# Kernel optimization log

Hardware: AMD Instinct MI355X
Metric: run time of the kernel (lower is better)

The kernel has to match this reference:

```python
import jax, jax.numpy as jnp
import numpy as np

WINDOW_SIZE = 11
SIGMA = 1.5
CHANNEL = 3
L = 2.0
C1 = (0.01 * L) ** 2
C2 = (0.03 * L) ** 2
WEIGHTS = jnp.asarray([0.0448, 0.2856, 0.3001, 0.2363, 0.1333], dtype=jnp.float32)


def _create_window(window_size=WINDOW_SIZE, channel=CHANNEL):
    x = jnp.arange(window_size, dtype=jnp.float32)
    g = jnp.exp(-((x - window_size // 2) ** 2) / (2.0 * SIGMA ** 2))
    g = g / g.sum()
    w2d = jnp.outer(g, g)  # (ws, ws)
    # depthwise kernel, OIHW with I=1, O=channel
    return jnp.broadcast_to(w2d[None, None], (channel, 1, window_size, window_size))


def _depthwise_conv(x, w):
    # x: (B,C,H,W), w: (C,1,kh,kw), groups=C, VALID padding
    return jax.lax.conv_general_dilated(
        x, w, window_strides=(1, 1), padding='VALID',
        feature_group_count=x.shape[1],
        dimension_numbers=('NCHW', 'OIHW', 'NCHW'))


def _ssim_level(img1, img2, window):
    mu1 = _depthwise_conv(img1, window)
    mu2 = _depthwise_conv(img2, window)
    mu1_sq = mu1 * mu1
    mu2_sq = mu2 * mu2
    mu1_mu2 = mu1 * mu2
    sigma1_sq = _depthwise_conv(img1 * img1, window) - mu1_sq
    sigma2_sq = _depthwise_conv(img2 * img2, window) - mu2_sq
    sigma12 = _depthwise_conv(img1 * img2, window) - mu1_mu2
    v1 = 2.0 * sigma12 + C2
    v2 = sigma1_sq + sigma2_sq + C2
    cs = jnp.mean(v1 / v2)
    ssim_map = (2.0 * mu1_mu2 + C1) * v1 / ((mu1_sq + mu2_sq + C1) * v2)
    return jnp.mean(ssim_map), cs


def _avg_pool2(x):
    b, c, h, w = x.shape
    return x.reshape(b, c, h // 2, 2, w // 2, 2).mean(axis=(3, 5))


def _msssim(img1, img2):
    window = _create_window()
    mssim, mcs = [], []
    for _ in range(WEIGHTS.shape[0]):
        sim, cs = _ssim_level(img1, img2, window)
        mssim.append(sim)
        mcs.append(cs)
        img1 = _avg_pool2(img1)
        img2 = _avg_pool2(img2)
    mssim = jnp.stack(mssim)
    mcs = jnp.stack(mcs)
    # normalize=True
    mssim = (mssim + 1.0) / 2.0
    mcs = (mcs + 1.0) / 2.0
    pow1 = mcs ** WEIGHTS
    pow2 = mssim ** WEIGHTS
    # faithful to source: prod over broadcast of pow1[:-1] * pow2[-1]
    return jnp.prod(pow1[:-1] * pow2[-1])


def setup_inputs() -> dict:
    key = jax.random.key(0)
    k1, k2 = jax.random.split(key)
    shape = (16, 3, 512, 512)
    output = jax.random.uniform(k1, shape, dtype=jnp.float32)
    gt = jax.random.uniform(k2, shape, dtype=jnp.float32)
    return {"output": output, "gt": gt}


def reference(output, gt):
    return 1.0 - _msssim(output, gt)
```

## Files before the change

kernel.cpp:

```cpp
#include <hip/hip_runtime.h>
#include <math.h>

typedef float vf2 __attribute__((ext_vector_type(2)));

__device__ __forceinline__ vf2 pk_fma(vf2 a, vf2 b, vf2 c) {
    vf2 d;
    asm("v_pk_fma_f32 %0, %1, %2, %3" : "=v"(d) : "v"(a), "v"(b), "v"(c));
    return d;
}
__device__ __forceinline__ vf2 pk_mul(vf2 a, vf2 b) {
    vf2 d;
    asm("v_pk_mul_f32 %0, %1, %2" : "=v"(d) : "v"(a), "v"(b));
    return d;
}
__device__ __forceinline__ vf2 pk_fma_blo(vf2 w, vf2 b, vf2 c) {
    vf2 d;
    asm("v_pk_fma_f32 %0, %1, %2, %3 op_sel_hi:[0,1,1]"
        : "=v"(d) : "v"(w), "v"(b), "v"(c));
    return d;
}
__device__ __forceinline__ vf2 pk_fma_bhi(vf2 w, vf2 b, vf2 c) {
    vf2 d;
    asm("v_pk_fma_f32 %0, %1, %2, %3 op_sel:[1,0,0] op_sel_hi:[1,1,1]"
        : "=v"(d) : "v"(w), "v"(b), "v"(c));
    return d;
}

#define L0_H 512
#define L0_HOUT 502
#define L0_HP 256
#define L0_SEG 64
#define L0_NCHUNK 7
#define ROWW 536
#define NQ 134
#define BUF_WORDS (11 * ROWW)
#define CARRY0 (2 * BUF_WORDS)
#define STREAM_WORDS (CARRY0 + 2 * ROWW)

__global__ __launch_bounds__(256)
void msssim_stream_l0(const float* __restrict__ img1,
                      const float* __restrict__ img2,
                      double* __restrict__ sums,
                      float* __restrict__ poolP, float* __restrict__ poolQ)
{
    __shared__ __align__(16) float buf[STREAM_WORDS];
    __shared__ float wred[4][2];

    const float gs[11] = {0.00102838f, 0.00759875f, 0.03600077f, 0.10936070f,
                          0.21300554f, 0.26601173f, 0.21300554f, 0.10936070f,
                          0.03600077f, 0.00759875f, 0.00102838f};

    const int tid = threadIdx.x;
    const int c0 = blockIdx.x * 256;
    const int oy0 = blockIdx.y * L0_SEG;
    const long long plane = (long long)blockIdx.z * L0_H * L0_H;
    const long long pplane = (long long)blockIdx.z * L0_HP * L0_HP;
    const bool colok = (c0 + tid) < L0_HOUT;

    const int par = tid & 1;
    vf2 wp[6];
    #pragma unroll
    for (int jq = 0; jq < 6; ++jq) {
        const int i0 = 2 * jq, i1 = 2 * jq + 1;
        const float we0 = (i0 < 11) ? gs[i0] : 0.f;
        const float wo0 = (i0 >= 1) ? gs[i0 - 1] : 0.f;
        const float we1 = (i1 < 11) ? gs[i1] : 0.f;
        const float wo1 = (i1 >= 1) ? gs[i1 - 1] : 0.f;
        wp[jq].x = par ? wo0 : we0;
        wp[jq].y = par ? wo1 : we1;
    }
    vf2 wgv[6];
    #pragma unroll
    for (int k = 0; k < 6; ++k) { wgv[k].x = gs[k]; wgv[k].y = gs[k]; }

    int rowS[6], colS[6], ldsoff[6], rHS[6];
    #pragma unroll
    for (int t = 0; t < 6; ++t) {
        const int s = tid + 256 * t;
        if (s < 11 * NQ) {
            const int r = s / NQ, q = s - NQ * r;
            rowS[t] = r;
            colS[t] = c0 + 2 * q;
            ldsoff[t] = r * ROWW + q * 4;
            rHS[t] = r * L0_H;
        } else { rowS[t] = -1; colS[t] = 0; ldsoff[t] = 0; rHS[t] = 0; }
    }

    float4 pf[6];
    auto prefetch = [&](int ybase) {
        const int yH = ybase * L0_H;
        #pragma unroll
        for (int t = 0; t < 6; ++t) {
            float2 a = make_float2(0.f, 0.f), b = make_float2(0.f, 0.f);
            if (rowS[t] >= 0) {
                const int y = ybase + rowS[t];
                if (y < L0_H && colS[t] < L0_H) {
                    const long long idx = plane + yH + rHS[t] + colS[t];
                    a = *(const float2*)(img1 + idx);
                    b = *(const float2*)(img2 + idx);
                }
            }
            pf[t] = make_float4(a.x + b.x, a.x - b.x, a.y + b.y, a.y - b.y);
        }
    };
    auto stage_write = [&](int base) {
        #pragma unroll
        for (int t = 0; t < 6; ++t)
            if (rowS[t] >= 0) *(float4*)&buf[base + ldsoff[t]] = pf[t];
    };

    prefetch(oy0);
    stage_write(0);
    __syncthreads();

    vf2 pd_pq[11], pd_sq[11];
    #pragma unroll
    for (int s = 0; s < 11; ++s) { pd_pq[s] = (vf2){0.f, 0.f}; pd_sq[s] = (vf2){0.f, 0.f}; }

    const int qb4 = (tid >> 1) * 4;
    const float C1 = 4.0e-4f, C2 = 3.6e-3f;
    float ssim_acc = 0.f, cs_acc = 0.f;

    for (int c = 0; c < L0_NCHUNK; ++c) {
        const int cs = oy0 + 11 * c;
        const bool more = (c + 1 < L0_NCHUNK);
        const int cb = (c & 1) * BUF_WORDS;
        const int nb = ((c + 1) & 1) * BUF_WORDS;

        if (more) prefetch(cs + 11);

        if (tid < 128) {
            const int px = (c0 >> 1) + tid;
            const int t4 = tid * 4;
            for (int jp = (cs & 1); jp + 1 <= 10; jp += 2) {
                const int py = (cs + jp) >> 1;
                if (py < L0_HP) {
                    const float4 v0 = *(const float4*)&buf[cb + jp * ROWW + t4];
                    const float4 v1 = *(const float4*)&buf[cb + (jp + 1) * ROWW + t4];
                    poolP[pplane + py * L0_HP + px] = 0.25f * (v0.x + v0.z + v1.x + v1.z);
                    poolQ[pplane + py * L0_HP + px] = 0.25f * (v0.y + v0.w + v1.y + v1.w);
                }
            }
            if (c > 0 && (cs & 1)) {
                const int py = (cs - 1) >> 1;
                if (py < L0_HP) {
                    const float4 v0 = *(const float4*)&buf[CARRY0 + ((c - 1) & 1) * ROWW + t4];
                    const float4 v1 = *(const float4*)&buf[cb + t4];
                    poolP[pplane + py * L0_HP + px] = 0.25f * (v0.x + v0.z + v1.x + v1.z);
                    poolQ[pplane + py * L0_HP + px] = 0.25f * (v0.y + v0.w + v1.y + v1.w);
                }
            }
        }
        if (((cs & 1) == 0) && more && tid < NQ) {
            *(float4*)&buf[CARRY0 + (c & 1) * ROWW + tid * 4] =
                *(const float4*)&buf[cb + 10 * ROWW + tid * 4];
        }

        #pragma unroll
        for (int j = 0; j < 11; ++j) {
            pd_pq[j] = (vf2){0.f, 0.f};
            pd_sq[j] = (vf2){0.f, 0.f};

            float4 q[6];
            const int rw = cb + j * ROWW + qb4;
            #pragma unroll
            for (int u = 0; u < 6; ++u) q[u] = *(const float4*)&buf[rw + 4 * u];

            vf2 hpq = {0.f, 0.f}, hsq = {0.f, 0.f};
            #pragma unroll
            for (int u = 0; u < 6; ++u) {
                const vf2 elo = {q[u].x, q[u].y};
                const vf2 ehi = {q[u].z, q[u].w};
                const vf2 slo = pk_mul(elo, elo);
                const vf2 shi = pk_mul(ehi, ehi);
                hpq = pk_fma_blo(wp[u], elo, hpq);
                hpq = pk_fma_bhi(wp[u], ehi, hpq);
                hsq = pk_fma_blo(wp[u], slo, hsq);
                hsq = pk_fma_bhi(wp[u], shi, hsq);
            }
            #pragma unroll
            for (int k = 0; k < 11; ++k) {
                const int s = (j - k + 11) % 11;
                const int m = (k <= 5) ? k : 10 - k;
                pd_pq[s] = pk_fma(wgv[m], hpq, pd_pq[s]);
                pd_sq[s] = pk_fma(wgv[m], hsq, pd_sq[s]);
            }
            const int yrel = 11 * c + j;
            if (yrel >= 10) {
                const int s = (j + 1) % 11;
                const int orow = yrel - 10;
                if (orow < L0_SEG && (oy0 + orow) < L0_HOUT && colok) {
                    const vf2 musq = pk_mul(pd_pq[s], pd_pq[s]);
                    const float sP = pd_sq[s].x - musq.x;
                    const float sQ = pd_sq[s].y - musq.y;
                    const float v1 = 0.5f * (sP - sQ) + C2;
                    const float v2 = 0.5f * (sP + sQ) + C2;
                    const float num1 = 0.5f * (musq.x - musq.y) + C1;
                    const float den1 = 0.5f * (musq.x + musq.y) + C1;
                    cs_acc += v1 * __builtin_amdgcn_rcpf(v2);
                    ssim_acc += num1 * v1 * __builtin_amdgcn_rcpf(den1 * v2);
                }
            }
        }

        if (more) stage_write(nb);
        __syncthreads();
    }

    #pragma unroll
    for (int off = 32; off > 0; off >>= 1) {
        ssim_acc += __shfl_down(ssim_acc, off);
        cs_acc   += __shfl_down(cs_acc, off);
    }
    const int wave = tid >> 6;
    if ((tid & 63) == 0) { wred[wave][0] = ssim_acc; wred[wave][1] = cs_acc; }
    __syncthreads();
    if (tid == 0) {
        atomicAdd(&sums[0], (double)(wred[0][0] + wred[1][0] + wred[2][0] + wred[3][0]));
        atomicAdd(&sums[5], (double)(wred[0][1] + wred[1][1] + wred[2][1] + wred[3][1]));
    }
}

#define TILE 32
#define IN_DIM 42
#define SCP 21
#define HALO 10
#define STAGE_WORDS (IN_DIM * SCP * 4)
#define SH 340
#define HB STAGE_WORDS
#define SMEM_WORDS (HB + 16 * SH)

__global__ __launch_bounds__(256)
void msssim_level_kernel(const float* __restrict__ src1,
                         const float* __restrict__ src2,
                         int H, int level, int tiles_per_seg, int pq_input,
                         double* __restrict__ sums,
                         float* __restrict__ pool1, float* __restrict__ pool2)
{
    __shared__ __align__(16) float smem[SMEM_WORDS];
    __shared__ float wred[4][2];

    const float g[11] = {0.00102838f, 0.00759875f, 0.03600077f, 0.10936070f,
                         0.21300554f, 0.26601173f, 0.21300554f, 0.10936070f,
                         0.03600077f, 0.00759875f, 0.00102838f};
    vf2 wg[11];
    #pragma unroll
    for (int k = 0; k < 11; ++k) { wg[k].x = g[k]; wg[k].y = g[k]; }

    const int tid = threadIdx.x;
    const int Hout = H - HALO;
    const int ntiles = (Hout + TILE - 1) / TILE;
    const int tstart = blockIdx.y * tiles_per_seg;
    const int tend = min(ntiles, tstart + tiles_per_seg);
    const int ox0 = blockIdx.x * TILE;
    const int Hp = H >> 1;
    const long long base = (long long)blockIdx.z * H * H;

    int rHS[4], rS[4], xS[4];
    #pragma unroll
    for (int t4 = 0; t4 < 4; ++t4) {
        const int s = tid + 256 * t4;
        if (s < IN_DIM * SCP) {
            const int r = s / SCP, cp = s - r * SCP;
            rS[t4] = r; rHS[t4] = r * H; xS[t4] = ox0 + 2 * cp;
        } else { rS[t4] = -1; rHS[t4] = 0; xS[t4] = 0; }
    }

    auto load_slot = [&](int t4, int ybase) -> float4 {
        float2 a = make_float2(0.f, 0.f), b = make_float2(0.f, 0.f);
        if (rS[t4] >= 0) {
            const int y = ybase + rS[t4], x = xS[t4];
            if (y < H && x < H) {
                const long long idx = base + (long long)ybase * H + rHS[t4] + x;
                a = *(const float2*)(src1 + idx);
                b = *(const float2*)(src2 + idx);
            }
        }
        if (pq_input) return make_float4(a.x, b.x, a.y, b.y);
        return make_float4(a.x + b.x, a.x - b.x, a.y + b.y, a.y - b.y);
    };

    float4 pref[4];
    {
        #pragma unroll
        for (int t4 = 0; t4 < 4; ++t4) pref[t4] = load_slot(t4, tstart * TILE);
        #pragma unroll
        for (int t4 = 0; t4 < 4; ++t4)
            if (rS[t4] >= 0) *(float4*)&smem[(tid + 256 * t4) * 4] = pref[t4];
    }
    __syncthreads();

    float ssim_acc = 0.f, cs_acc = 0.f;

    for (int tt = tstart; tt < tend; ++tt) {
        const int ty0 = tt * TILE;
        const bool more = (tt + 1 < tend);

        if (more) {
            #pragma unroll
            for (int t4 = 0; t4 < 4; ++t4) pref[t4] = load_slot(t4, ty0 + TILE);
        }

        if (pool1 != nullptr) {
            const int pr = tid >> 4, pc = tid & 15;
            const int py = (ty0 >> 1) + pr, px = (ox0 >> 1) + pc;
            if (py < Hp && px < Hp) {
                const float4 v0 = *(const float4*)&smem[(2 * pr * SCP + pc) * 4];
                const float4 v1 = *(const float4*)&smem[((2 * pr + 1) * SCP + pc) * 4];
                const long long ob = (long long)blockIdx.z * Hp * Hp + (long long)py * Hp + px;
                pool1[ob] = 0.25f * (v0.x + v0.z + v1.x + v1.z);
                pool2[ob] = 0.25f * (v0.y + v0.w + v1.y + v1.w);
            }
        }

        float4 hA[3], hBv[3];
        #pragma unroll
        for (int t = 0; t < 3; ++t) {
            const int p = tid + 256 * t;
            if (p < IN_DIM * 16) {
                const int r = p >> 4, m = p & 15;
                vf2 Apq = {0.f, 0.f}, Asq = {0.f, 0.f};
                vf2 Bpq = {0.f, 0.f}, Bsq = {0.f, 0.f};
                #pragma unroll
                for (int jj = 0; jj < 6; ++jj) {
                    const float4 v = *(const float4*)&smem[(r * SCP + m + jj) * 4];
                    const vf2 lo = {v.x, v.y};
                    const vf2 hi = {v.z, v.w};
                    const vf2 losq = pk_mul(lo, lo);
                    const vf2 hisq = pk_mul(hi, hi);
                    Apq = pk_fma(wg[2 * jj], lo, Apq);
                    Asq = pk_fma(wg[2 * jj], losq, Asq);
                    if (jj >= 1) {
                        Bpq = pk_fma(wg[2 * jj - 1], lo, Bpq);
                        Bsq = pk_fma(wg[2 * jj - 1], losq, Bsq);
                    }
                    if (jj <= 4) {
                        Apq = pk_fma(wg[2 * jj + 1], hi, Apq);
                        Asq = pk_fma(wg[2 * jj + 1], hisq, Asq);
                    }
                    Bpq = pk_fma(wg[2 * jj], hi, Bpq);
                    Bsq = pk_fma(wg[2 * jj], hisq, Bsq);
                }
                hA[t]  = make_float4(Apq.x, Apq.y, Asq.x, Asq.y);
                hBv[t] = make_float4(Bpq.x, Bpq.y, Bsq.x, Bsq.y);
            }
        }
        __syncthreads();

        #pragma unroll
        for (int t = 0; t < 3; ++t) {
            const int p = tid + 256 * t;
            if (p < IN_DIM * 16) {
                const int r = p >> 4, m = p & 15;
                const int hb = HB + m * SH + r * 8;
                *(float4*)&smem[hb]     = hA[t];
                *(float4*)&smem[hb + 4] = hBv[t];
            }
        }
        if (more) {
            #pragma unroll
            for (int t4 = 0; t4 < 4; ++t4)
                if (rS[t4] >= 0) *(float4*)&smem[(tid + 256 * t4) * 4] = pref[t4];
        }
        __syncthreads();

        const int tx = tid & 31, rg = tid >> 5;
        const int r0 = rg * 4;
        const int m = tx >> 1, par = tx & 1;
        const int hb = HB + m * SH + par * 4;

        vf2 accPQ[4], accSQ[4];
        #pragma unroll
        for (int o = 0; o < 4; ++o) {
            accPQ[o] = (vf2){0.f, 0.f};
            accSQ[o] = (vf2){0.f, 0.f};
        }
        #pragma unroll
        for (int i = 0; i < 14; ++i) {
            const float4 h4 = *(const float4*)&smem[hb + (r0 + i) * 8];
            const vf2 ppq = {h4.x, h4.y};
            const vf2 psq = {h4.z, h4.w};
            #pragma unroll
            for (int o = 0; o < 4; ++o) {
                const int k = i - o;
                if (k >= 0 && k <= 10) {
                    accPQ[o] = pk_fma(wg[k], ppq, accPQ[o]);
                    accSQ[o] = pk_fma(wg[k], psq, accSQ[o]);
                }
            }
        }

        const float C1 = 4.0e-4f;
        const float C2 = 3.6e-3f;
        const int ox = ox0 + tx;
        #pragma unroll
        for (int o = 0; o < 4; ++o) {
            const int oy = ty0 + r0 + o;
            if (oy < Hout && ox < Hout) {
                const vf2 musq = pk_mul(accPQ[o], accPQ[o]);
                const float sP = accSQ[o].x - musq.x;
                const float sQ = accSQ[o].y - musq.y;
                const float v1 = 0.5f * (sP - sQ) + C2;
                const float v2 = 0.5f * (sP + sQ) + C2;
                const float num1 = 0.5f * (musq.x - musq.y) + C1;
                const float den1 = 0.5f * (musq.x + musq.y) + C1;
                cs_acc += v1 * __builtin_amdgcn_rcpf(v2);
                ssim_acc += num1 * v1 * __builtin_amdgcn_rcpf(den1 * v2);
            }
        }
    }

    #pragma unroll
    for (int off = 32; off > 0; off >>= 1) {
        ssim_acc += __shfl_down(ssim_acc, off);
        cs_acc   += __shfl_down(cs_acc, off);
    }
    const int wave = tid >> 6;
    if ((tid & 63) == 0) { wred[wave][0] = ssim_acc; wred[wave][1] = cs_acc; }
    __syncthreads();
    if (tid == 0) {
        const float s = wred[0][0] + wred[1][0] + wred[2][0] + wred[3][0];
        const float c = wred[0][1] + wred[1][1] + wred[2][1] + wred[3][1];
        atomicAdd(&sums[level],     (double)s);
        atomicAdd(&sums[5 + level], (double)c);
    }
}

__global__ void msssim_final_kernel(const double* __restrict__ sums,
                                    float* __restrict__ out)
{
    if (threadIdx.x == 0 && blockIdx.x == 0) {
        const double W[5] = {0.0448, 0.2856, 0.3001, 0.2363, 0.1333};
        const int Houts[5] = {502, 246, 118, 54, 22};
        double mssim[5], mcs[5];
        for (int l = 0; l < 5; ++l) {
            const double cnt = 48.0 * (double)Houts[l] * (double)Houts[l];
            mssim[l] = (sums[l]     / cnt + 1.0) * 0.5;
            mcs[l]   = (sums[5 + l] / cnt + 1.0) * 0.5;
        }
        const double p2 = pow(mssim[4], W[4]);
        double prod = 1.0;
        for (int l = 0; l < 4; ++l) prod *= pow(mcs[l], W[l]) * p2;
        out[0] = (float)(1.0 - prod);
    }
}

extern "C" void kernel_launch(void* const* d_in, const int* in_sizes, int n_in,
                              void* d_out, int out_size, void* d_ws, size_t ws_size,
                              hipStream_t stream)
{
    const float* img1 = (const float*)d_in[0];
    const float* img2 = (const float*)d_in[1];
    float* out = (float*)d_out;
    (void)in_sizes; (void)n_in; (void)out_size; (void)ws_size;

    char* ws = (char*)d_ws;
    double* sums = (double*)ws;
    float* X1 = (float*)(ws + 256);
    float* X2 = X1 + 3145728;
    float* Y1 = X2 + 3145728;
    float* Y2 = Y1 + 786432;

    hipMemsetAsync(sums, 0, 10 * sizeof(double), stream);

    hipLaunchKernelGGL(msssim_stream_l0, dim3(2, 8, 48), dim3(256), 0, stream,
                       img1, img2, sums, X1, X2);

    auto launch_level = [&](const float* a, const float* b, int H, int level,
                            int segs, float* pa, float* pb) {
        const int Hout = H - HALO;
        const int strips = (Hout + TILE - 1) / TILE;
        const int ntiles = (Hout + TILE - 1) / TILE;
        const int tps = (ntiles + segs - 1) / segs;
        dim3 grid(strips, segs, 48);
        hipLaunchKernelGGL(msssim_level_kernel, grid, dim3(256), 0, stream,
                           a, b, H, level, tps, 1, sums, pa, pb);
    };

    launch_level(X1, X2, 256, 1, 2, Y1, Y2);
    launch_level(Y1, Y2, 128, 2, 4, X1, X2);
    launch_level(X1, X2, 64, 3, 2, Y1, Y2);
    launch_level(Y1, Y2, 32, 4, 1, nullptr, nullptr);

    hipLaunchKernelGGL(msssim_final_kernel, dim3(1), dim3(64), 0, stream, sums, out);
}
```

Measured before the change: 139.8 us.

## Precompute pyramid in one pool kernel and fuse levels 1-4 into one launch

A new kernel builds all downsampled levels (128, 64, 32) from the level-1 buffers in one pass per plane using LDS. The four per-level SSIM launches are then merged into a single launch whose blocks pick their level, strip and segment from a flat block index. The goal is to remove the serial dependency chain and the launch gaps between the small levels, so that the tiny levels run alongside level 1 and fill the GPU. The cost is an extra pool kernel with only 96 blocks, which may run with low occupancy, plus re-reading the level-1 data.

```diff
diff --git a/kernel.cpp b/kernel.cpp
--- a/kernel.cpp
+++ b/kernel.cpp
@@ -221,6 +221,44 @@
     }
 }
 
+__global__ __launch_bounds__(256)
+void msssim_pool_cascade(const float* __restrict__ X1, const float* __restrict__ X2,
+                         float* __restrict__ Y1, float* __restrict__ Y2,
+                         float* __restrict__ Z1, float* __restrict__ Z2,
+                         float* __restrict__ W1, float* __restrict__ W2)
+{
+    __shared__ float ys[16384];
+    __shared__ float zs[4096];
+    const int tid = threadIdx.x;
+    const int plane = blockIdx.x >> 1;
+    const int img = blockIdx.x & 1;
+    const float* src = (img ? X2 : X1) + (long long)plane * 65536;
+    float* yg = (img ? Y2 : Y1) + (long long)plane * 16384;
+    float* zg = (img ? Z2 : Z1) + (long long)plane * 4096;
+    float* wg = (img ? W2 : W1) + (long long)plane * 1024;
+
+    for (int i = tid; i < 16384; i += 256) {
+        const int y = i >> 7, x = i & 127;
+        const float2 t0 = *(const float2*)&src[(2 * y) * 256 + 2 * x];
+        const float2 t1 = *(const float2*)&src[(2 * y + 1) * 256 + 2 * x];
+        const float v = 0.25f * (t0.x + t0.y + t1.x + t1.y);
+        ys[i] = v; yg[i] = v;
+    }
+    __syncthreads();
+    for (int i = tid; i < 4096; i += 256) {
+        const int y = i >> 6, x = i & 63;
+        const float v = 0.25f * (ys[(2 * y) * 128 + 2 * x] + ys[(2 * y) * 128 + 2 * x + 1]
+                               + ys[(2 * y + 1) * 128 + 2 * x] + ys[(2 * y + 1) * 128 + 2 * x + 1]);
+        zs[i] = v; zg[i] = v;
+    }
+    __syncthreads();
+    for (int i = tid; i < 1024; i += 256) {
+        const int y = i >> 5, x = i & 31;
+        wg[i] = 0.25f * (zs[(2 * y) * 64 + 2 * x] + zs[(2 * y) * 64 + 2 * x + 1]
+                       + zs[(2 * y + 1) * 64 + 2 * x] + zs[(2 * y + 1) * 64 + 2 * x + 1]);
+    }
+}
+
 #define TILE 32
 #define IN_DIM 42
 #define SCP 21
@@ -231,14 +269,31 @@
 #define SMEM_WORDS (HB + 16 * SH)
 
 __global__ __launch_bounds__(256)
-void msssim_level_kernel(const float* __restrict__ src1,
-                         const float* __restrict__ src2,
-                         int H, int level, int tiles_per_seg, int pq_input,
-                         double* __restrict__ sums,
-                         float* __restrict__ pool1, float* __restrict__ pool2)
+void msssim_fused_levels(const float* __restrict__ X1, const float* __restrict__ X2,
+                         const float* __restrict__ Y1, const float* __restrict__ Y2,
+                         const float* __restrict__ Z1, const float* __restrict__ Z2,
+                         const float* __restrict__ W1, const float* __restrict__ W2,
+                         double* __restrict__ sums)
 {
     __shared__ __align__(16) float smem[SMEM_WORDS];
     __shared__ float wred[4][2];
+
+    const int bid = blockIdx.x;
+    const float *src1, *src2;
+    int H, level, strip, seg, plane, tps;
+    if (bid < 768) {
+        level = 1; H = 256; src1 = X1; src2 = X2; tps = 4;
+        const int r = bid;        plane = r >> 4; const int t = r & 15; strip = t & 7; seg = t >> 3;
+    } else if (bid < 1536) {
+        level = 2; H = 128; src1 = Y1; src2 = Y2; tps = 1;
+        const int r = bid - 768;  plane = r >> 4; const int t = r & 15; strip = t & 3; seg = t >> 2;
+    } else if (bid < 1728) {
+        level = 3; H = 64;  src1 = Z1; src2 = Z2; tps = 1;
+        const int r = bid - 1536; plane = r >> 2; const int t = r & 3;  strip = t & 1; seg = t >> 1;
+    } else {
+        level = 4; H = 32;  src1 = W1; src2 = W2; tps = 1;
+        plane = bid - 1728; strip = 0; seg = 0;
+    }
 
     const float g[11] = {0.00102838f, 0.00759875f, 0.03600077f, 0.10936070f,
                          0.21300554f, 0.26601173f, 0.21300554f, 0.10936070f,
@@ -250,11 +305,10 @@
     const int tid = threadIdx.x;
     const int Hout = H - HALO;
     const int ntiles = (Hout + TILE - 1) / TILE;
-    const int tstart = blockIdx.y * tiles_per_seg;
-    const int tend = min(ntiles, tstart + tiles_per_seg);
-    const int ox0 = blockIdx.x * TILE;
-    const int Hp = H >> 1;
-    const long long base = (long long)blockIdx.z * H * H;
+    const int tstart = seg * tps;
+    const int tend = min(ntiles, tstart + tps);
+    const int ox0 = strip * TILE;
+    const long long base = (long long)plane * H * H;
 
     int rHS[4], rS[4], xS[4];
     #pragma unroll
@@ -276,8 +330,7 @@
                 b = *(const float2*)(src2 + idx);
             }
         }
-        if (pq_input) return make_float4(a.x, b.x, a.y, b.y);
-        return make_float4(a.x + b.x, a.x - b.x, a.y + b.y, a.y - b.y);
+        return make_float4(a.x, b.x, a.y, b.y);
     };
 
     float4 pref[4];
@@ -299,18 +352,6 @@
         if (more) {
             #pragma unroll
             for (int t4 = 0; t4 < 4; ++t4) pref[t4] = load_slot(t4, ty0 + TILE);
-        }
-
-        if (pool1 != nullptr) {
-            const int pr = tid >> 4, pc = tid & 15;
-            const int py = (ty0 >> 1) + pr, px = (ox0 >> 1) + pc;
-            if (py < Hp && px < Hp) {
-                const float4 v0 = *(const float4*)&smem[(2 * pr * SCP + pc) * 4];
-                const float4 v1 = *(const float4*)&smem[((2 * pr + 1) * SCP + pc) * 4];
-                const long long ob = (long long)blockIdx.z * Hp * Hp + (long long)py * Hp + px;
-                pool1[ob] = 0.25f * (v0.x + v0.z + v1.x + v1.z);
-                pool2[ob] = 0.25f * (v0.y + v0.w + v1.y + v1.w);
-            }
         }
 
         float4 hA[3], hBv[3];
@@ -460,27 +501,21 @@
     float* X2 = X1 + 3145728;
     float* Y1 = X2 + 3145728;
     float* Y2 = Y1 + 786432;
+    float* Z1 = Y2 + 786432;
+    float* Z2 = Z1 + 196608;
+    float* W1 = Z2 + 196608;
+    float* W2 = W1 + 49152;
 
     hipMemsetAsync(sums, 0, 10 * sizeof(double), stream);
 
     hipLaunchKernelGGL(msssim_stream_l0, dim3(2, 8, 48), dim3(256), 0, stream,
                        img1, img2, sums, X1, X2);
 
-    auto launch_level = [&](const float* a, const float* b, int H, int level,
-                            int segs, float* pa, float* pb) {
-        const int Hout = H - HALO;
-        const int strips = (Hout + TILE - 1) / TILE;
-        const int ntiles = (Hout + TILE - 1) / TILE;
-        const int tps = (ntiles + segs - 1) / segs;
-        dim3 grid(strips, segs, 48);
-        hipLaunchKernelGGL(msssim_level_kernel, grid, dim3(256), 0, stream,
-                           a, b, H, level, tps, 1, sums, pa, pb);
-    };
-
-    launch_level(X1, X2, 256, 1, 2, Y1, Y2);
-    launch_level(Y1, Y2, 128, 2, 4, X1, X2);
-    launch_level(X1, X2, 64, 3, 2, Y1, Y2);
-    launch_level(Y1, Y2, 32, 4, 1, nullptr, nullptr);
+    hipLaunchKernelGGL(msssim_pool_cascade, dim3(96), dim3(256), 0, stream,
+                       X1, X2, Y1, Y2, Z1, Z2, W1, W2);
+
+    hipLaunchKernelGGL(msssim_fused_levels, dim3(1776), dim3(256), 0, stream,
+                       X1, X2, Y1, Y2, Z1, Z2, W1, W2, sums);
 
     hipLaunchKernelGGL(msssim_final_kernel, dim3(1), dim3(64), 0, stream, sums, out);
 }
```

After: 131.8 us. 5.7% less time.
